# Performance work log

Hardware: AMD Instinct MI355X
Metric: run time of the kernel (lower is better)

## Reference

```python
import jax, jax.numpy as jnp
import numpy as np

V, H, FAST, SLOW = 32000, 256, 64, 256
B, T = 32, 1024
THRESH = 0.3
NEG = -1e9


def setup_inputs() -> dict:
    key = jax.random.key(0)
    ks = jax.random.split(key, 16)
    s = 0.02
    return {
        "seq":   jax.random.randint(ks[0], (B, T), 0, V),
        "embed": jax.random.normal(ks[1], (V, H), jnp.float32) * s,
        "W1": jax.random.normal(ks[2], (H, 2 * H), jnp.float32) * s,
        "b1": jnp.zeros((2 * H,), jnp.float32),
        "W2": jax.random.normal(ks[3], (2 * H, H), jnp.float32) * s,
        "b2": jnp.zeros((H,), jnp.float32),
        "gamma": jnp.ones((H,), jnp.float32),
        "beta":  jnp.zeros((H,), jnp.float32),
        "Wg": jax.random.normal(ks[4], (H, 1), jnp.float32) * s,
        "bg": jnp.zeros((1,), jnp.float32),
        "Wd": jax.random.normal(ks[5], (H, 1), jnp.float32) * s,
        "bd": jnp.zeros((1,), jnp.float32),
        "Wq": jax.random.normal(ks[6], (H, H), jnp.float32) * s,
        "bq": jnp.zeros((H,), jnp.float32),
        "Wo": jax.random.normal(ks[7], (H, V), jnp.float32) * s,
        "bo": jnp.zeros((V,), jnp.float32),
    }


def _layer_norm(x, g, b, eps=1e-5):
    mu = x.mean(-1, keepdims=True)
    var = ((x - mu) ** 2).mean(-1, keepdims=True)
    return (x - mu) * jax.lax.rsqrt(var + eps) * g + b


def _writer(h, Wg, bg, Wd, bd):
    """Vectorized-over-batch LRU writer with learned demotion; scan over time."""
    Bn = h.shape[0]
    init = (
        jnp.zeros((Bn, FAST, H), h.dtype),   # fast_mem
        jnp.zeros((Bn, SLOW, H), h.dtype),   # slow_mem
        jnp.zeros((Bn, FAST), jnp.int32),    # fast_age
        jnp.zeros((Bn, SLOW), jnp.int32),    # slow_age
        jnp.zeros((Bn, FAST), bool),         # fast_used
        jnp.zeros((Bn, SLOW), bool),         # slow_used
    )

    def step(st, tok_h):
        fm, sm, fa, sa, fu, su = st
        ws = jax.nn.sigmoid(tok_h @ Wg + bg)[:, 0]          # [B]
        fa = fa + fu.astype(jnp.int32)
        sa = sa + su.astype(jnp.int32)
        write = ws >= 0.4                                    # torch skips if < 0.4
        tok = jax.lax.stop_gradient(tok_h)                   # .detach() in torch

        free_f = ~fu                                         # [B,FAST]
        has_free = jnp.any(free_f, axis=1)                   # [B]
        sl = jnp.argmax(free_f, axis=1)                      # first free fast slot

        ds = (fm @ Wd + bd)[..., 0]                          # [B,FAST] demotion scores
        dem = jnp.argmin(ds, axis=1)                         # [B]
        dh = jnp.take_along_axis(fm, dem[:, None, None], axis=1)[:, 0]  # [B,H]

        free_s = ~su
        has_free_s = jnp.any(free_s, axis=1)
        ss = jnp.where(has_free_s, jnp.argmax(free_s, axis=1), jnp.argmax(sa, axis=1))

        fidx = jnp.where(has_free, sl, dem)                  # fast write slot
        sel_f = jax.nn.one_hot(fidx, FAST, dtype=bool) & write[:, None]
        do_slow = write & ~has_free                          # demotion happens
        sel_s = jax.nn.one_hot(ss, SLOW, dtype=bool) & do_slow[:, None]

        # slow write (demoted value) uses fm BEFORE the fast overwrite
        sm = jnp.where(sel_s[:, :, None], dh[:, None, :], sm)
        sa = jnp.where(sel_s, 0, sa)
        su = su | sel_s

        fm = jnp.where(sel_f[:, :, None], tok[:, None, :], fm)
        fa = jnp.where(sel_f, 0, fa)
        fu = fu | sel_f
        return (fm, sm, fa, sa, fu, su), None

    tokens = jnp.swapaxes(h[:, : h.shape[1] - 3], 0, 1)      # [T-3, B, H]
    (fm, sm, fa, sa, fu, su), _ = jax.lax.scan(step, init, tokens)
    return fm, sm, fu.astype(h.dtype), su.astype(h.dtype)


def reference(seq, embed, W1, b1, W2, b2, gamma, beta, Wg, bg, Wd, bd, Wq, bq, Wo, bo):
    h0 = embed[seq]                                          # [B,T,H]
    ff = jnp.maximum(h0 @ W1 + b1, 0.0) @ W2 + b2
    h = _layer_norm(h0 + ff, gamma, beta)

    fm, sm, fmask, smask = _writer(h, Wg, bg, Wd, bd)

    q = h[:, -1, :] @ Wq + bq                                # [B,H]
    f_scores = jnp.einsum("bfd,bd->bf", fm, q)
    f_scores = jnp.where(fmask == 0, NEG, f_scores)
    f_attn = jax.nn.softmax(f_scores, axis=-1)
    f_ctx = jnp.einsum("bf,bfd->bd", f_attn, fm)
    max_attn = f_attn.max(axis=-1)

    s_scores = jnp.einsum("bsd,bd->bs", sm, q)
    s_scores = jnp.where(smask == 0, NEG, s_scores)
    s_attn = jax.nn.softmax(s_scores, axis=-1)
    s_ctx = jnp.einsum("bs,bsd->bd", s_attn, sm)

    need_slow = (max_attn < THRESH).astype(h.dtype)          # [B]
    ctx = f_ctx + need_slow[:, None] * s_ctx
    logits = ctx @ Wo + bo
    return logits, need_slow
```

## Files before the change

kernel.cpp:

```cpp
#include <hip/hip_runtime.h>
#include <hip/hip_bf16.h>
#include <cstdint>

#define NEGV -1e9f

typedef __attribute__((ext_vector_type(8))) short short8v;
typedef __attribute__((ext_vector_type(4))) float f32x4;

union U8 {
  unsigned u[4];
  short8v v;
};

__device__ __forceinline__ float wred_sum(float v) {
#pragma unroll
  for (int o = 32; o; o >>= 1) v += __shfl_xor(v, o);
  return v;
}
__device__ __forceinline__ float wred_max(float v) {
#pragma unroll
  for (int o = 32; o; o >>= 1) v = fmaxf(v, __shfl_xor(v, o));
  return v;
}
template <int CTRL>
__device__ __forceinline__ float dpp_fadd(float x) {
  int xi = __float_as_int(x);
  int yi = __builtin_amdgcn_update_dpp(xi, xi, CTRL, 0xF, 0xF, false);
  return x + __int_as_float(yi);
}
__device__ __forceinline__ float dpp_sum63(float v) {
  v = dpp_fadd<0xB1>(v);
  v = dpp_fadd<0x4E>(v);
  v = dpp_fadd<0x141>(v);
  v = dpp_fadd<0x140>(v);
  v = dpp_fadd<0x142>(v);
  v = dpp_fadd<0x143>(v);
  return v;
}
__device__ __forceinline__ float dpp_sum16(float v) {
  v = dpp_fadd<0xB1>(v);
  v = dpp_fadd<0x4E>(v);
  v = dpp_fadd<0x141>(v);
  v = dpp_fadd<0x140>(v);
  return v;
}

__device__ __forceinline__ ushort bf16hi(float x) {
  unsigned u = __float_as_uint(x);
  unsigned r = u + 0x7FFFu + ((u >> 16) & 1u);
  return (ushort)(r >> 16);
}
__device__ __forceinline__ float bf16tof(ushort u) {
  return __uint_as_float(((unsigned)u) << 16);
}
__device__ __forceinline__ void split8(const float* xs, uint4& hv, uint4& lv) {
  unsigned h[8], l[8];
#pragma unroll
  for (int j = 0; j < 8; ++j) {
    const ushort hh = bf16hi(xs[j]);
    h[j] = hh;
    l[j] = bf16hi(xs[j] - bf16tof(hh));
  }
  hv = make_uint4(h[0] | (h[1] << 16), h[2] | (h[3] << 16),
                  h[4] | (h[5] << 16), h[6] | (h[7] << 16));
  lv = make_uint4(l[0] | (l[1] << 16), l[2] | (l[3] << 16),
                  l[4] | (l[5] << 16), l[6] | (l[7] << 16));
}

__device__ __forceinline__ void gload_lds16(const void* g, void* l) {
  __builtin_amdgcn_global_load_lds(
      (const __attribute__((address_space(1))) unsigned int*)g,
      (__attribute__((address_space(3))) unsigned int*)l, 16, 0, 0);
}

__global__ __launch_bounds__(256) void wprep2_k(const float* __restrict__ W,
                                                char* __restrict__ Wti, int K,
                                                int N) {
  __shared__ float tile[32][33];
  const int k0 = blockIdx.x * 32, n0 = blockIdx.y * 32;
  const int r = threadIdx.x >> 5, c = threadIdx.x & 31;
#pragma unroll
  for (int i = 0; i < 4; ++i)
    tile[r + i * 8][c] = W[(size_t)(k0 + r + i * 8) * N + n0 + c];
  __syncthreads();
  if (threadIdx.x < 128) {
    const int gn = threadIdx.x & 31, gk = threadIdx.x >> 5;
    float xs[8];
#pragma unroll
    for (int i = 0; i < 8; ++i) xs[i] = tile[gk * 8 + i][gn];
    uint4 hv, lv;
    split8(xs, hv, lv);
    char* dst = Wti + (size_t)(n0 + gn) * K * 4 + (k0 >> 5) * 128 + gk * 16;
    *(uint4*)dst = hv;
    *(uint4*)(dst + 64) = lv;
  }
}

__global__ __launch_bounds__(256) void aprep_k(const int* __restrict__ seq,
                                               const float* __restrict__ embed,
                                               char* __restrict__ aembi) {
  const int row = blockIdx.x * 8 + (threadIdx.x >> 5);
  const int sl = threadIdx.x & 31;
  const float* ap = embed + (size_t)seq[row] * 256 + sl * 8;
  const float4 x0 = *(const float4*)ap;
  const float4 x1 = *(const float4*)(ap + 4);
  const float xs[8] = {x0.x, x0.y, x0.z, x0.w, x1.x, x1.y, x1.z, x1.w};
  uint4 hv, lv;
  split8(xs, hv, lv);
  char* dst = aembi + (size_t)row * 1024 + (sl >> 2) * 128 + (sl & 3) * 16;
  *(uint4*)dst = hv;
  *(uint4*)(dst + 64) = lv;
}

__global__ __launch_bounds__(512, 2) void gemm1i_k(
    const char* __restrict__ aembi, const char* __restrict__ w1ti,
    const float* __restrict__ bias, unsigned* __restrict__ outp) {
  __shared__ alignas(16) ushort A[4096];
  __shared__ alignas(16) ushort B[16384];
  const int tid = threadIdx.x;
  const int m0 = blockIdx.x * 64, n0 = blockIdx.y * 256;
  const int lane = tid & 63, w = tid >> 6;
  const int wm = (w >> 2) * 32, wn = (w & 3) * 64;
  const int r15 = lane & 15, khalf = lane >> 4;

  f32x4 acc[2][4];
#pragma unroll
  for (int i = 0; i < 2; ++i)
#pragma unroll
    for (int j = 0; j < 4; ++j) acc[i][j] = (f32x4){0.f, 0.f, 0.f, 0.f};

#pragma unroll 1
  for (int s = 0; s < 8; ++s) {
    const size_t sb = (size_t)s * 128;
    {
      const int cb = w * 64;
      const int c = cb + lane;
      const int row = c >> 3;
      const int lc = (c & 7) ^ (row & 7);
      gload_lds16(aembi + (size_t)(m0 + row) * 1024 + sb + lc * 16,
                  &A[cb * 8]);
    }
#pragma unroll
    for (int i = 0; i < 4; ++i) {
      const int cb = i * 512 + w * 64;
      const int c = cb + lane;
      const int row = c >> 3;
      const int lc = (c & 7) ^ (row & 7);
      gload_lds16(w1ti + (size_t)(n0 + row) * 1024 + sb + lc * 16,
                  &B[cb * 8]);
    }
    __syncthreads();
    short8v ahf[2], alf[2], bhf[4], blf[4];
#pragma unroll
    for (int t = 0; t < 2; ++t) {
      const int ra = wm + t * 16 + r15;
      ahf[t] = *(const short8v*)&A[(ra * 8 + (khalf ^ (ra & 7))) * 8];
      alf[t] = *(const short8v*)&A[(ra * 8 + ((4 | khalf) ^ (ra & 7))) * 8];
    }
#pragma unroll
    for (int t = 0; t < 4; ++t) {
      const int rb = wn + t * 16 + r15;
      bhf[t] = *(const short8v*)&B[(rb * 8 + (khalf ^ (rb & 7))) * 8];
      blf[t] = *(const short8v*)&B[(rb * 8 + ((4 | khalf) ^ (rb & 7))) * 8];
    }
#pragma unroll
    for (int mi = 0; mi < 2; ++mi)
#pragma unroll
      for (int ni = 0; ni < 4; ++ni) {
        acc[mi][ni] = __builtin_amdgcn_mfma_f32_16x16x32_bf16(
            ahf[mi], bhf[ni], acc[mi][ni], 0, 0, 0);
        acc[mi][ni] = __builtin_amdgcn_mfma_f32_16x16x32_bf16(
            ahf[mi], blf[ni], acc[mi][ni], 0, 0, 0);
        acc[mi][ni] = __builtin_amdgcn_mfma_f32_16x16x32_bf16(
            alf[mi], bhf[ni], acc[mi][ni], 0, 0, 0);
      }
    __syncthreads();
  }
#pragma unroll
  for (int ni = 0; ni < 4; ++ni) {
    const int n = n0 + wn + ni * 16 + r15;
    const float bv = bias[n];
#pragma unroll
    for (int mi = 0; mi < 2; ++mi) {
      const int mbase = m0 + wm + mi * 16 + khalf * 4;
#pragma unroll
      for (int j = 0; j < 4; ++j) {
        const float t = fmaxf(acc[mi][ni][j] + bv, 0.f);
        const ushort h = bf16hi(t);
        const ushort l = bf16hi(t - bf16tof(h));
        outp[(size_t)(mbase + j) * 512 + n] = (unsigned)h | ((unsigned)l << 16);
      }
    }
  }
}

__global__ __launch_bounds__(512, 2) void gemm2i_k(
    const unsigned* __restrict__ Ap, const char* __restrict__ w2ti,
    const float* __restrict__ b2, const int* __restrict__ seq,
    const float* __restrict__ embed, const float* __restrict__ gamma,
    const float* __restrict__ beta, const float* __restrict__ Wg,
    const float* __restrict__ bg, const float* __restrict__ Wd,
    const float* __restrict__ bd, float* __restrict__ X,
    int* __restrict__ wbit, float* __restrict__ dsc) {
  __shared__ alignas(16) unsigned Apk[2048];
  __shared__ alignas(16) ushort B[16384];
  __shared__ float par0[64][4], par1[64][4], gpar[64][4], dpar[64][4];
  __shared__ float g_s[256], be_s[256], wg_s[256], wd_s[256], b2_s[256];
  __shared__ int sidx[64];
  const int tid = threadIdx.x;
  const int m0 = blockIdx.x * 64;
  if (tid < 64) sidx[tid] = seq[m0 + tid];
  if (tid >= 256) {
    const int c = tid - 256;
    g_s[c] = gamma[c];
    be_s[c] = beta[c];
    wg_s[c] = Wg[c];
    wd_s[c] = Wd[c];
    b2_s[c] = b2[c];
  }
  const int lane = tid & 63, w = tid >> 6;
  const int wm = (w >> 2) * 32, wn = (w & 3) * 64;
  const int r15 = lane & 15, khalf = lane >> 4;

  f32x4 acc[2][4];
#pragma unroll
  for (int i = 0; i < 2; ++i)
#pragma unroll
    for (int j = 0; j < 4; ++j) acc[i][j] = (f32x4){0.f, 0.f, 0.f, 0.f};

#pragma unroll 1
  for (int s = 0; s < 16; ++s) {
    {
      const int cb = w * 64;
      const int c = cb + lane;
      const int row = c >> 3;
      const int lc = (c & 7) ^ (row & 7);
      gload_lds16(Ap + (size_t)(m0 + row) * 512 + s * 32 + lc * 4,
                  &Apk[cb * 4]);
    }
    const size_t sb = (size_t)s * 128;
#pragma unroll
    for (int i = 0; i < 4; ++i) {
      const int cb = i * 512 + w * 64;
      const int c = cb + lane;
      const int row = c >> 3;
      const int lc = (c & 7) ^ (row & 7);
      gload_lds16(w2ti + (size_t)row * 2048 + sb + lc * 16, &B[cb * 8]);
    }
    __syncthreads();
    short8v ahf[2], alf[2], bhf[4], blf[4];
#pragma unroll
    for (int t = 0; t < 2; ++t) {
      const int ra = wm + t * 16 + r15;
      const int r7 = ra & 7;
      const uint4 ua = *(const uint4*)&Apk[(ra * 8 + ((khalf * 2) ^ r7)) * 4];
      const uint4 ub =
          *(const uint4*)&Apk[(ra * 8 + ((khalf * 2 + 1) ^ r7)) * 4];
      U8 vh, vl;
      vh.u[0] = (ua.x & 0xffffu) | (ua.y << 16);
      vl.u[0] = (ua.x >> 16) | (ua.y & 0xffff0000u);
      vh.u[1] = (ua.z & 0xffffu) | (ua.w << 16);
      vl.u[1] = (ua.z >> 16) | (ua.w & 0xffff0000u);
      vh.u[2] = (ub.x & 0xffffu) | (ub.y << 16);
      vl.u[2] = (ub.x >> 16) | (ub.y & 0xffff0000u);
      vh.u[3] = (ub.z & 0xffffu) | (ub.w << 16);
      vl.u[3] = (ub.z >> 16) | (ub.w & 0xffff0000u);
      ahf[t] = vh.v;
      alf[t] = vl.v;
    }
#pragma unroll
    for (int t = 0; t < 4; ++t) {
      const int rb = wn + t * 16 + r15;
      bhf[t] = *(const short8v*)&B[(rb * 8 + (khalf ^ (rb & 7))) * 8];
      blf[t] = *(const short8v*)&B[(rb * 8 + ((4 | khalf) ^ (rb & 7))) * 8];
    }
#pragma unroll
    for (int mi = 0; mi < 2; ++mi)
#pragma unroll
      for (int ni = 0; ni < 4; ++ni) {
        acc[mi][ni] = __builtin_amdgcn_mfma_f32_16x16x32_bf16(
            ahf[mi], bhf[ni], acc[mi][ni], 0, 0, 0);
        acc[mi][ni] = __builtin_amdgcn_mfma_f32_16x16x32_bf16(
            ahf[mi], blf[ni], acc[mi][ni], 0, 0, 0);
        acc[mi][ni] = __builtin_amdgcn_mfma_f32_16x16x32_bf16(
            alf[mi], bhf[ni], acc[mi][ni], 0, 0, 0);
      }
    __syncthreads();
  }

  float mu_r[2][4];
#pragma unroll
  for (int mi = 0; mi < 2; ++mi)
#pragma unroll
    for (int j = 0; j < 4; ++j) {
      const int rowl = wm + mi * 16 + khalf * 4 + j;
      const float* ep = embed + (size_t)sidx[rowl] * 256;
#pragma unroll
      for (int ni = 0; ni < 4; ++ni) {
        const int col = wn + ni * 16 + r15;
        float t = acc[mi][ni][j] + b2_s[col];
        acc[mi][ni][j] = t + ep[col];
      }
      float s = (acc[mi][0][j] + acc[mi][1][j]) + (acc[mi][2][j] + acc[mi][3][j]);
      s = dpp_sum16(s);
      if (r15 == 0) par0[rowl][w & 3] = s;
    }
  __syncthreads();
#pragma unroll
  for (int mi = 0; mi < 2; ++mi)
#pragma unroll
    for (int j = 0; j < 4; ++j) {
      const int rowl = wm + mi * 16 + khalf * 4 + j;
      const float mu = ((par0[rowl][0] + par0[rowl][1]) +
                        (par0[rowl][2] + par0[rowl][3])) * (1.f / 256.f);
      mu_r[mi][j] = mu;
      const float d0 = acc[mi][0][j] - mu, d1 = acc[mi][1][j] - mu;
      const float d2 = acc[mi][2][j] - mu, d3 = acc[mi][3][j] - mu;
      float vv = (d0 * d0 + d1 * d1) + (d2 * d2 + d3 * d3);
      vv = dpp_sum16(vv);
      if (r15 == 0) par1[rowl][w & 3] = vv;
    }
  __syncthreads();
#pragma unroll
  for (int mi = 0; mi < 2; ++mi)
#pragma unroll
    for (int j = 0; j < 4; ++j) {
      const int rowl = wm + mi * 16 + khalf * 4 + j;
      const float mu = mu_r[mi][j];
      const float var = ((par1[rowl][0] + par1[rowl][1]) +
                         (par1[rowl][2] + par1[rowl][3])) * (1.f / 256.f);
      const float rstd = 1.f / sqrtf(var + 1e-5f);
      float ys[4], gw[4], dw[4];
#pragma unroll
      for (int ni = 0; ni < 4; ++ni) {
        const int col = wn + ni * 16 + r15;
        const float y = (acc[mi][ni][j] - mu) * rstd * g_s[col] + be_s[col];
        X[(size_t)(m0 + rowl) * 256 + col] = y;
        ys[ni] = y;
        gw[ni] = wg_s[col];
        dw[ni] = wd_s[col];
      }
      float gp = (ys[0] * gw[0] + ys[1] * gw[1]) + (ys[2] * gw[2] + ys[3] * gw[3]);
      float dp = (ys[0] * dw[0] + ys[1] * dw[1]) + (ys[2] * dw[2] + ys[3] * dw[3]);
      gp = dpp_sum16(gp);
      dp = dpp_sum16(dp);
      if (r15 == 0) {
        gpar[rowl][w & 3] = gp;
        dpar[rowl][w & 3] = dp;
      }
    }
  __syncthreads();
  if (tid < 64) {
    const int row = tid;
    const float gs = ((gpar[row][0] + gpar[row][1]) +
                      (gpar[row][2] + gpar[row][3])) + bg[0];
    const float dsv = ((dpar[row][0] + dpar[row][1]) +
                       (dpar[row][2] + dpar[row][3])) + bd[0];
    float sig;
    if (gs >= 0.f) {
      sig = 1.f / (1.f + expf(-gs));
    } else {
      const float e2 = expf(gs);
      sig = e2 / (1.f + e2);
    }
    wbit[m0 + row] = (sig >= 0.4f) ? 1 : 0;
    dsc[m0 + row] = dsv;
  }
}

__global__ __launch_bounds__(1024) void select_k(
    const int* __restrict__ wbit, const float* __restrict__ dsc,
    int* __restrict__ ftok, int* __restrict__ stok, int* __restrict__ cnt) {
  const int b = blockIdx.x;
  const int tid = threadIdx.x;
  const int lane = tid & 63, wv = tid >> 6;
  __shared__ unsigned long long skey[1024];
  __shared__ int stokl[1024];
  __shared__ int wavecnt[16];
  __shared__ int waveoff[17];
  __shared__ int fcnt_s[16], scnt_s[16];
  __shared__ int foff[16], soff[16];

  const int t = tid;
  int flag = 0;
  float d = 0.f;
  if (t < 1021) {
    flag = wbit[b * 1024 + t];
    d = dsc[b * 1024 + t];
  }
  const unsigned long long m = __ballot(flag != 0);
  if (lane == 0) wavecnt[wv] = __popcll(m);
  __syncthreads();
  if (tid == 0) {
    int acc = 0;
    for (int i = 0; i < 16; ++i) { waveoff[i] = acc; acc += wavecnt[i]; }
    waveoff[16] = acc;
  }
  __syncthreads();
  const int W = waveoff[16];
  if (flag) {
    unsigned u = __float_as_uint(d);
    u = (u & 0x80000000u) ? ~u : (u | 0x80000000u);
    const int w = waveoff[wv] + __popcll(m & ((1ull << lane) - 1ull));
    skey[w] = ((unsigned long long)u << 32) | (unsigned)w;
    stokl[w] = t;
  }
  __syncthreads();

  const int K = W - 64;
  const int end2 = max(0, W - 257);
  const int endAll = W - 1;
  bool fastf = false, slowf = false;
  if (tid < W) {
    const unsigned long long ki = skey[tid];
    int r1 = 0, r2 = 0;
    int j = 0;
    for (; j < end2; ++j) {
      const int lt = skey[j] < ki;
      r1 += lt;
      r2 += lt;
    }
    for (; j < endAll; ++j) r1 += (skey[j] < ki);
    const bool isLast = (tid == W - 1);
    const bool inEK = (!isLast) && (r1 < K);
    const bool inE2 = (tid < end2) && (r2 < K - 256);
    fastf = isLast || (!isLast && r1 >= K);
    slowf = inEK && !inE2;
  }

  const unsigned long long mf = __ballot(fastf);
  const unsigned long long ms = __ballot(slowf);
  if (lane == 0) { fcnt_s[wv] = __popcll(mf); scnt_s[wv] = __popcll(ms); }
  __syncthreads();
  if (tid == 0) {
    int a = 0, c = 0;
    for (int i = 0; i < 16; ++i) {
      foff[i] = a; a += fcnt_s[i];
      soff[i] = c; c += scnt_s[i];
    }
  }
  __syncthreads();
  if (fastf) {
    const int p = foff[wv] + __popcll(mf & ((1ull << lane) - 1ull));
    ftok[b * 64 + p] = stokl[tid];
  }
  if (slowf) {
    const int p = soff[wv] + __popcll(ms & ((1ull << lane) - 1ull));
    stok[b * 256 + p] = stokl[tid];
  }
  if (tid == 0) {
    cnt[b * 2] = W;
    cnt[b * 2 + 1] = max(K, 0);
  }
}

__global__ __launch_bounds__(1024) void attn2_k(
    const float* __restrict__ X, const float* __restrict__ Wq,
    const float* __restrict__ bq, const int* __restrict__ ftok,
    const int* __restrict__ stok, const int* __restrict__ cnt,
    float* __restrict__ ctx, float* __restrict__ needs_out) {
  const int b = blockIdx.x;
  const int tid = threadIdx.x;
  const int lane = tid & 63, wv = tid >> 6;
  __shared__ float hl[256], q[256];
  __shared__ float qpart[4][256];
  __shared__ float sc_f[64], at_f[64];
  __shared__ float sc_s[256], at_s[256];
  __shared__ int ft[64], st[256];
  __shared__ float redm[4], reds[4];
  __shared__ float needs_s;
  __shared__ float cpart[16][256];
  const float* Xb = X + (size_t)b * 1024 * 256;
  if (tid < 256) hl[tid] = Xb[(size_t)1023 * 256 + tid];
  else if (tid < 320) ft[tid - 256] = ftok[b * 64 + tid - 256];
  else if (tid < 576) st[tid - 320] = stok[b * 256 + tid - 320];
  __syncthreads();
  const int nf = min(cnt[b * 2], 64);
  const int ns = min(cnt[b * 2 + 1], 256);

  {
    const int col = tid & 255, kc = tid >> 8;
    float a = 0.f;
    const float* wp = Wq + (size_t)(kc * 64) * 256 + col;
#pragma unroll 4
    for (int k = 0; k < 64; ++k) a = fmaf(hl[kc * 64 + k], wp[(size_t)k * 256], a);
    qpart[kc][col] = a;
  }
  __syncthreads();
  if (tid < 256)
    q[tid] = ((qpart[0][tid] + qpart[1][tid]) + qpart[2][tid]) + qpart[3][tid] +
             bq[tid];
  __syncthreads();

  const float4 qq = *(const float4*)(q + lane * 4);
#pragma unroll 2
  for (int i = 0; i < 20; ++i) {
    const int r = wv + 16 * i;
    bool valid;
    int tok;
    if (r < 64) { valid = r < nf; tok = valid ? ft[r] : 0; }
    else        { valid = (r - 64) < ns; tok = valid ? st[r - 64] : 0; }
    float sc = NEGV;
    if (valid) {
      const float4 xr = *(const float4*)(Xb + (size_t)tok * 256 + lane * 4);
      float p = (xr.x * qq.x + xr.y * qq.y) + (xr.z * qq.z + xr.w * qq.w);
      sc = dpp_sum63(p);
    }
    if (lane == 63) {
      if (r < 64) sc_f[r] = sc;
      else sc_s[r - 64] = sc;
    }
  }
  __syncthreads();

  if (wv < 4) {
    float s = sc_s[tid];
    float mx = wred_max(s);
    if (lane == 0) redm[wv] = mx;
  } else if (wv == 8) {
    float s = sc_f[lane];
    float mx = wred_max(s);
    float e = expf(s - mx);
    float sm = wred_sum(e);
    float a = e / sm;
    at_f[lane] = a;
    float ma = wred_max(a);
    if (lane == 0) needs_s = (ma < 0.3f) ? 1.f : 0.f;
  }
  __syncthreads();
  if (wv < 4) {
    float s = sc_s[tid];
    float mx = fmaxf(fmaxf(redm[0], redm[1]), fmaxf(redm[2], redm[3]));
    float e = expf(s - mx);
    float sm = wred_sum(e);
    if (lane == 0) reds[wv] = sm;
    at_s[tid] = e;
  }
  __syncthreads();
  if (tid < 256) {
    float sm = (reds[0] + reds[1]) + (reds[2] + reds[3]);
    at_s[tid] = at_s[tid] / sm;
  }
  __syncthreads();

  const float needs = needs_s;
  float4 cp = {0.f, 0.f, 0.f, 0.f};
#pragma unroll 2
  for (int i = 0; i < 20; ++i) {
    const int r = wv + 16 * i;
    bool valid;
    int tok;
    float a;
    if (r < 64) { valid = r < nf; tok = valid ? ft[r] : 0; a = at_f[r]; }
    else {
      valid = (r - 64) < ns;
      tok = valid ? st[r - 64] : 0;
      a = needs * at_s[r - 64];
    }
    if (valid) {
      const float4 xr = *(const float4*)(Xb + (size_t)tok * 256 + lane * 4);
      cp.x = fmaf(a, xr.x, cp.x);
      cp.y = fmaf(a, xr.y, cp.y);
      cp.z = fmaf(a, xr.z, cp.z);
      cp.w = fmaf(a, xr.w, cp.w);
    }
  }
  *(float4*)&cpart[wv][lane * 4] = cp;
  __syncthreads();
  if (tid < 256) {
    float c = 0.f;
#pragma unroll
    for (int w = 0; w < 16; ++w) c += cpart[w][tid];
    ctx[b * 256 + tid] = c;
  }
  if (tid == 0) needs_out[b] = needs;
}

__global__ __launch_bounds__(256) void logits5_k(
    const float* __restrict__ ctx, const float* __restrict__ Wo,
    const float* __restrict__ bo, float* __restrict__ out) {
  __shared__ float cs[256 * 8];
  const int tid = threadIdx.x;
  const int b0 = blockIdx.y * 8;
  for (int i = tid; i < 2048; i += 256) {
    int bb = i & 7, hh = i >> 3;
    cs[hh * 8 + bb] = ctx[(b0 + bb) * 256 + hh];
  }
  __syncthreads();
  const int v = blockIdx.x * 256 + tid;
  float acc[8] = {0.f, 0.f, 0.f, 0.f, 0.f, 0.f, 0.f, 0.f};
  for (int h0 = 0; h0 < 256; h0 += 16) {
    float wv[16];
#pragma unroll
    for (int u = 0; u < 16; ++u) wv[u] = Wo[(size_t)(h0 + u) * 32000 + v];
#pragma unroll
    for (int u = 0; u < 16; ++u) {
      const float4 c0 = *(const float4*)&cs[(h0 + u) * 8];
      const float4 c1 = *(const float4*)&cs[(h0 + u) * 8 + 4];
      acc[0] = fmaf(c0.x, wv[u], acc[0]);
      acc[1] = fmaf(c0.y, wv[u], acc[1]);
      acc[2] = fmaf(c0.z, wv[u], acc[2]);
      acc[3] = fmaf(c0.w, wv[u], acc[3]);
      acc[4] = fmaf(c1.x, wv[u], acc[4]);
      acc[5] = fmaf(c1.y, wv[u], acc[5]);
      acc[6] = fmaf(c1.z, wv[u], acc[6]);
      acc[7] = fmaf(c1.w, wv[u], acc[7]);
    }
  }
  const float bv = bo[v];
#pragma unroll
  for (int bb = 0; bb < 8; ++bb)
    out[(size_t)(b0 + bb) * 32000 + v] = acc[bb] + bv;
}

extern "C" void kernel_launch(void* const* d_in, const int* in_sizes, int n_in,
                              void* d_out, int out_size, void* d_ws,
                              size_t ws_size, hipStream_t stream) {
  const int* seq = (const int*)d_in[0];
  const float* embed = (const float*)d_in[1];
  const float* W1 = (const float*)d_in[2];
  const float* b1 = (const float*)d_in[3];
  const float* W2 = (const float*)d_in[4];
  const float* b2 = (const float*)d_in[5];
  const float* gamma = (const float*)d_in[6];
  const float* beta = (const float*)d_in[7];
  const float* Wg = (const float*)d_in[8];
  const float* bg = (const float*)d_in[9];
  const float* Wd = (const float*)d_in[10];
  const float* bd = (const float*)d_in[11];
  const float* Wq = (const float*)d_in[12];
  const float* bq = (const float*)d_in[13];
  const float* Wo = (const float*)d_in[14];
  const float* bo = (const float*)d_in[15];
  float* out = (float*)d_out;

  char* wsb = (char*)d_ws;
  char* w1ti = wsb;
  char* w2ti = wsb + 524288;
  int* wbit = (int*)(wsb + 1048576);
  float* dscp = (float*)(wsb + 1179648);
  int* ftokp = (int*)(wsb + 1310720);
  int* stokp = (int*)(wsb + 1318912);
  int* cntp = (int*)(wsb + 1351680);
  float* ctxp = (float*)(wsb + 1351936);
  const size_t base = 1384704;

  const int nch = (ws_size >= (size_t)137000000) ? 1 : 2;
  const int rows = 32768 / nch;
  const size_t aesz = (size_t)rows * 1024;
  const size_t actsz = (size_t)rows * 512 * 4;
  char* aembi = wsb + base;
  unsigned* act1p = (unsigned*)(wsb + base + aesz);
  float* X = (float*)(wsb + base + aesz + actsz);

  dim3 blk(256);
  wprep2_k<<<dim3(8, 16), blk, 0, stream>>>(W1, w1ti, 256, 512);
  wprep2_k<<<dim3(16, 8), blk, 0, stream>>>(W2, w2ti, 512, 256);

  for (int c = 0; c < nch; ++c) {
    const int* seqc = seq + c * rows;
    aprep_k<<<dim3(rows / 8), blk, 0, stream>>>(seqc, embed, aembi);
    gemm1i_k<<<dim3(rows / 64, 2), dim3(512), 0, stream>>>(aembi, w1ti, b1,
                                                           act1p);
    gemm2i_k<<<dim3(rows / 64), dim3(512), 0, stream>>>(
        act1p, w2ti, b2, seqc, embed, gamma, beta, Wg, bg, Wd, bd,
        X + (size_t)c * rows * 256, wbit + c * rows, dscp + c * rows);
  }

  select_k<<<32, dim3(1024), 0, stream>>>(wbit, dscp, ftokp, stokp, cntp);
  attn2_k<<<32, dim3(1024), 0, stream>>>(X, Wq, bq, ftokp, stokp, cntp, ctxp,
                                         out + (size_t)32 * 32000);
  logits5_k<<<dim3(125, 4), blk, 0, stream>>>(ctxp, Wo, bo, out);
}
```

Baseline: 165.7 us.

## Fuse embedding gather/split into GEMM1 and merge select with attention kernel

The separate aprep kernel, which gathered embedding rows and split them into hi/lo bf16 pairs in a workspace buffer, is removed. GEMM1 now gathers the embedding rows and splits them directly into its swizzled LDS A tile on each k-step. The select and attention kernels are also merged into one kernel that keeps token lists in shared memory, which drops two launches and the 32MB intermediate buffer. In exchange, the A operand is now recomputed for each of the two N-blocks, and the loads go through registers instead of direct-to-LDS transfers, with only half the threads loading A.

```diff
diff --git a/kernel.cpp b/kernel.cpp
--- a/kernel.cpp
+++ b/kernel.cpp
@@ -96,29 +96,17 @@
   }
 }
 
-__global__ __launch_bounds__(256) void aprep_k(const int* __restrict__ seq,
-                                               const float* __restrict__ embed,
-                                               char* __restrict__ aembi) {
-  const int row = blockIdx.x * 8 + (threadIdx.x >> 5);
-  const int sl = threadIdx.x & 31;
-  const float* ap = embed + (size_t)seq[row] * 256 + sl * 8;
-  const float4 x0 = *(const float4*)ap;
-  const float4 x1 = *(const float4*)(ap + 4);
-  const float xs[8] = {x0.x, x0.y, x0.z, x0.w, x1.x, x1.y, x1.z, x1.w};
-  uint4 hv, lv;
-  split8(xs, hv, lv);
-  char* dst = aembi + (size_t)row * 1024 + (sl >> 2) * 128 + (sl & 3) * 16;
-  *(uint4*)dst = hv;
-  *(uint4*)(dst + 64) = lv;
-}
-
-__global__ __launch_bounds__(512, 2) void gemm1i_k(
-    const char* __restrict__ aembi, const char* __restrict__ w1ti,
-    const float* __restrict__ bias, unsigned* __restrict__ outp) {
+__global__ __launch_bounds__(512, 2) void gemm1g_k(
+    const int* __restrict__ seq, const float* __restrict__ embed,
+    const char* __restrict__ w1ti, const float* __restrict__ bias,
+    unsigned* __restrict__ outp) {
   __shared__ alignas(16) ushort A[4096];
   __shared__ alignas(16) ushort B[16384];
+  __shared__ int sidx[64];
   const int tid = threadIdx.x;
   const int m0 = blockIdx.x * 64, n0 = blockIdx.y * 256;
+  if (tid < 64) sidx[tid] = seq[m0 + tid];
+  __syncthreads();
   const int lane = tid & 63, w = tid >> 6;
   const int wm = (w >> 2) * 32, wn = (w & 3) * 64;
   const int r15 = lane & 15, khalf = lane >> 4;
@@ -132,13 +120,17 @@
 #pragma unroll 1
   for (int s = 0; s < 8; ++s) {
     const size_t sb = (size_t)s * 128;
-    {
-      const int cb = w * 64;
-      const int c = cb + lane;
-      const int row = c >> 3;
-      const int lc = (c & 7) ^ (row & 7);
-      gload_lds16(aembi + (size_t)(m0 + row) * 1024 + sb + lc * 16,
-                  &A[cb * 8]);
+    if (tid < 256) {
+      const int row = tid >> 2, q = tid & 3;
+      const float* ap = embed + (size_t)sidx[row] * 256 + s * 32 + q * 8;
+      const float4 x0 = *(const float4*)ap;
+      const float4 x1 = *(const float4*)(ap + 4);
+      const float xs[8] = {x0.x, x0.y, x0.z, x0.w, x1.x, x1.y, x1.z, x1.w};
+      uint4 hv, lv;
+      split8(xs, hv, lv);
+      const int r7 = row & 7;
+      *(uint4*)&A[(row * 8 + (q ^ r7)) * 8] = hv;
+      *(uint4*)&A[(row * 8 + ((4 | q) ^ r7)) * 8] = lv;
     }
 #pragma unroll
     for (int i = 0; i < 4; ++i) {
@@ -368,9 +360,11 @@
   }
 }
 
-__global__ __launch_bounds__(1024) void select_k(
+__global__ __launch_bounds__(1024) void selattn_k(
     const int* __restrict__ wbit, const float* __restrict__ dsc,
-    int* __restrict__ ftok, int* __restrict__ stok, int* __restrict__ cnt) {
+    const float* __restrict__ X, const float* __restrict__ Wq,
+    const float* __restrict__ bq, float* __restrict__ ctx,
+    float* __restrict__ needs_out) {
   const int b = blockIdx.x;
   const int tid = threadIdx.x;
   const int lane = tid & 63, wv = tid >> 6;
@@ -380,6 +374,14 @@
   __shared__ int waveoff[17];
   __shared__ int fcnt_s[16], scnt_s[16];
   __shared__ int foff[16], soff[16];
+  __shared__ int ft[64], st[256];
+  __shared__ float hl[256], q[256];
+  __shared__ float qpart[4][256];
+  __shared__ float sc_f[64], at_f[64];
+  __shared__ float sc_s[256], at_s[256];
+  __shared__ float redm[4], reds[4];
+  __shared__ float needs_s;
+  __shared__ float cpart[16][256];
 
   const int t = tid;
   int flag = 0;
@@ -442,41 +444,18 @@
   __syncthreads();
   if (fastf) {
     const int p = foff[wv] + __popcll(mf & ((1ull << lane) - 1ull));
-    ftok[b * 64 + p] = stokl[tid];
+    ft[p] = stokl[tid];
   }
   if (slowf) {
     const int p = soff[wv] + __popcll(ms & ((1ull << lane) - 1ull));
-    stok[b * 256 + p] = stokl[tid];
-  }
-  if (tid == 0) {
-    cnt[b * 2] = W;
-    cnt[b * 2 + 1] = max(K, 0);
-  }
-}
-
-__global__ __launch_bounds__(1024) void attn2_k(
-    const float* __restrict__ X, const float* __restrict__ Wq,
-    const float* __restrict__ bq, const int* __restrict__ ftok,
-    const int* __restrict__ stok, const int* __restrict__ cnt,
-    float* __restrict__ ctx, float* __restrict__ needs_out) {
-  const int b = blockIdx.x;
-  const int tid = threadIdx.x;
-  const int lane = tid & 63, wv = tid >> 6;
-  __shared__ float hl[256], q[256];
-  __shared__ float qpart[4][256];
-  __shared__ float sc_f[64], at_f[64];
-  __shared__ float sc_s[256], at_s[256];
-  __shared__ int ft[64], st[256];
-  __shared__ float redm[4], reds[4];
-  __shared__ float needs_s;
-  __shared__ float cpart[16][256];
+    st[p] = stokl[tid];
+  }
+  const int nf = min(W, 64);
+  const int ns = min(max(K, 0), 256);
+
   const float* Xb = X + (size_t)b * 1024 * 256;
   if (tid < 256) hl[tid] = Xb[(size_t)1023 * 256 + tid];
-  else if (tid < 320) ft[tid - 256] = ftok[b * 64 + tid - 256];
-  else if (tid < 576) st[tid - 320] = stok[b * 256 + tid - 320];
-  __syncthreads();
-  const int nf = min(cnt[b * 2], 64);
-  const int ns = min(cnt[b * 2 + 1], 256);
+  __syncthreads();
 
   {
     const int col = tid & 255, kc = tid >> 8;
@@ -639,19 +618,14 @@
   char* w2ti = wsb + 524288;
   int* wbit = (int*)(wsb + 1048576);
   float* dscp = (float*)(wsb + 1179648);
-  int* ftokp = (int*)(wsb + 1310720);
-  int* stokp = (int*)(wsb + 1318912);
-  int* cntp = (int*)(wsb + 1351680);
-  float* ctxp = (float*)(wsb + 1351936);
-  const size_t base = 1384704;
-
-  const int nch = (ws_size >= (size_t)137000000) ? 1 : 2;
+  float* ctxp = (float*)(wsb + 1310720);
+  const size_t base = 1343488;
+
+  const int nch = (ws_size >= (size_t)105000000) ? 1 : 2;
   const int rows = 32768 / nch;
-  const size_t aesz = (size_t)rows * 1024;
   const size_t actsz = (size_t)rows * 512 * 4;
-  char* aembi = wsb + base;
-  unsigned* act1p = (unsigned*)(wsb + base + aesz);
-  float* X = (float*)(wsb + base + aesz + actsz);
+  unsigned* act1p = (unsigned*)(wsb + base);
+  float* X = (float*)(wsb + base + actsz);
 
   dim3 blk(256);
   wprep2_k<<<dim3(8, 16), blk, 0, stream>>>(W1, w1ti, 256, 512);
@@ -659,16 +633,14 @@
 
   for (int c = 0; c < nch; ++c) {
     const int* seqc = seq + c * rows;
-    aprep_k<<<dim3(rows / 8), blk, 0, stream>>>(seqc, embed, aembi);
-    gemm1i_k<<<dim3(rows / 64, 2), dim3(512), 0, stream>>>(aembi, w1ti, b1,
-                                                           act1p);
+    gemm1g_k<<<dim3(rows / 64, 2), dim3(512), 0, stream>>>(seqc, embed, w1ti,
+                                                           b1, act1p);
     gemm2i_k<<<dim3(rows / 64), dim3(512), 0, stream>>>(
         act1p, w2ti, b2, seqc, embed, gamma, beta, Wg, bg, Wd, bd,
         X + (size_t)c * rows * 256, wbit + c * rows, dscp + c * rows);
   }
 
-  select_k<<<32, dim3(1024), 0, stream>>>(wbit, dscp, ftokp, stokp, cntp);
-  attn2_k<<<32, dim3(1024), 0, stream>>>(X, Wq, bq, ftokp, stokp, cntp, ctxp,
-                                         out + (size_t)32 * 32000);
+  selattn_k<<<32, dim3(1024), 0, stream>>>(wbit, dscp, X, Wq, bq, ctxp,
+                                           out + (size_t)32 * 32000);
   logits5_k<<<dim3(125, 4), blk, 0, stream>>>(ctxp, Wo, bo, out);
 }
```

Result: faster. 156.5 us (-5.5%).
